# Optimization experiments

Measured on AMD Instinct MI355X. Metric: run time of the kernel, lower is better.

## Reference

```python
import jax, jax.numpy as jnp
import numpy as np

N = 100000      # nodes
E = 1600000     # edges (avg degree 16)
EP = 500000     # pos/neg scored edges
DIN, DH, DOUT = 128, 128, 64


def setup_inputs() -> dict:
    key = jax.random.key(0)
    ks = jax.random.split(key, 8)
    x = jax.random.normal(ks[0], (N, DIN), jnp.float32)
    edge_index = jax.random.randint(ks[1], (2, E), 0, N)
    pos_edge_index = jax.random.randint(ks[2], (2, EP), 0, N)
    neg_edge_index = jax.random.randint(ks[3], (2, EP), 0, N)
    s = lambda k, sh: jax.random.normal(k, sh, jnp.float32) * 0.05
    return dict(
        x=x, edge_index=edge_index,
        pos_edge_index=pos_edge_index, neg_edge_index=neg_edge_index,
        W_l0=s(ks[4], (DIN, DH)), b_l0=jnp.zeros((DH,), jnp.float32), W_r0=s(ks[5], (DIN, DH)),
        W_l1=s(ks[6], (DH, DOUT)), b_l1=jnp.zeros((DOUT,), jnp.float32), W_r1=s(ks[7], (DH, DOUT)),
    )


def sage_conv(h, src, dst, W_l, b_l, W_r):
    # PyG SAGEConv (mean aggr): out_i = W_l @ mean_{j in N(i)} h_j + b_l + W_r @ h_i
    msg = h[src]                                                   # [E, d] gather
    agg = jax.ops.segment_sum(msg, dst, num_segments=h.shape[0])   # [N, d]
    deg = jax.ops.segment_sum(jnp.ones((src.shape[0],), h.dtype), dst, num_segments=h.shape[0])
    mean = agg / jnp.maximum(deg, 1.0)[:, None]
    return mean @ W_l + b_l + h @ W_r


def reference(x, edge_index, pos_edge_index, neg_edge_index,
              W_l0, b_l0, W_r0, W_l1, b_l1, W_r1):
    src, dst = edge_index[0], edge_index[1]
    h = sage_conv(x, src, dst, W_l0, b_l0, W_r0)
    h = jax.nn.relu(h)          # dropout is identity in eval mode
    h = sage_conv(h, src, dst, W_l1, b_l1, W_r1)
    pos_scores = (h[pos_edge_index[0]] * h[pos_edge_index[1]]).sum(axis=1)
    neg_scores = (h[neg_edge_index[0]] * h[neg_edge_index[1]]).sum(axis=1)
    return (pos_scores, neg_scores)
```

## Files before the change

kernel.cpp:

```cpp
#include <hip/hip_runtime.h>

#define NN 100000
#define EE 1600000
#define EPE 500000
#define NBINS 196
#define BCAP 12288
#define EPB 2048
#define NB1 782

typedef short bf8_t __attribute__((ext_vector_type(8)));
typedef float f4_t  __attribute__((ext_vector_type(4)));

__device__ __forceinline__ unsigned short f2bf(float f) {
    unsigned u = __float_as_uint(f);
    unsigned r = (u + 0x7fffu + ((u >> 16) & 1u)) >> 16;
    return (unsigned short)r;
}
__device__ __forceinline__ float bfl(unsigned u) { return __uint_as_float(u << 16); }
__device__ __forceinline__ float bfh(unsigned u) { return __uint_as_float(u & 0xffff0000u); }

__global__ __launch_bounds__(256) void binpass1_k(
    const int* __restrict__ src, const int* __restrict__ dst,
    int* __restrict__ bin_cnt, int* __restrict__ binbuf)
{
    __shared__ int cnt_l[NBINS];
    __shared__ int base_l[NBINS];
    int tid = threadIdx.x;
    int e0 = blockIdx.x * EPB;
    for (int i = tid; i < NBINS; i += 256) cnt_l[i] = 0;
    __syncthreads();

    int pk[8];
    #pragma unroll
    for (int i = 0; i < 8; ++i) {
        int e = e0 + tid + i * 256;
        pk[i] = -1;
        if (e < EE) {
            int b = dst[e] >> 9;
            int r = atomicAdd(&cnt_l[b], 1);
            pk[i] = (b << 16) | r;
        }
    }
    __syncthreads();
    for (int i = tid; i < NBINS; i += 256)
        base_l[i] = atomicAdd(&bin_cnt[i], cnt_l[i]);
    __syncthreads();

    #pragma unroll
    for (int i = 0; i < 8; ++i) {
        int e = e0 + tid + i * 256;
        if (e >= EE) continue;
        int b = pk[i] >> 16, r = pk[i] & 0xFFFF;
        int d = dst[e], s = src[e];
        binbuf[b * BCAP + base_l[b] + r] = ((d & 511) << 17) | s;
    }
}

__global__ __launch_bounds__(256) void binpass2_k(
    const int* __restrict__ binbuf, const int* __restrict__ bin_cnt,
    int* __restrict__ csr, int* __restrict__ row_ptr, float* __restrict__ invd)
{
    __shared__ int deg_l[512];
    __shared__ int off_l[512];
    __shared__ int cur_l[512];
    __shared__ int s[256];
    int tid = threadIdx.x;
    int b = blockIdx.x;
    int lo = b << 9;
    int n_here = min(512, NN - lo);

    int bc = (tid < NBINS) ? bin_cnt[tid] : 0;
    s[tid] = bc;
    __syncthreads();
    #pragma unroll
    for (int off = 1; off < 256; off <<= 1) {
        int t = (tid >= off) ? s[tid - off] : 0;
        __syncthreads();
        s[tid] += t;
        __syncthreads();
    }
    int base = (b == 0) ? 0 : s[b - 1];
    int cnt = bin_cnt[b];
    const int* bb = binbuf + b * BCAP;
    __syncthreads();

    deg_l[tid] = 0; deg_l[tid + 256] = 0;
    __syncthreads();
    for (int i = tid; i < cnt; i += 256)
        atomicAdd(&deg_l[bb[i] >> 17], 1);
    __syncthreads();

    int a0 = deg_l[2 * tid], a1 = deg_l[2 * tid + 1];
    s[tid] = a0 + a1;
    __syncthreads();
    #pragma unroll
    for (int off = 1; off < 256; off <<= 1) {
        int t = (tid >= off) ? s[tid - off] : 0;
        __syncthreads();
        s[tid] += t;
        __syncthreads();
    }
    int excl = s[tid] - (a0 + a1);
    off_l[2 * tid] = excl;
    off_l[2 * tid + 1] = excl + a0;
    cur_l[2 * tid] = excl;
    cur_l[2 * tid + 1] = excl + a0;
    __syncthreads();

    for (int j = tid; j < n_here; j += 256) {
        row_ptr[lo + j] = base + off_l[j];
        invd[lo + j] = 1.0f / fmaxf((float)deg_l[j], 1.0f);
    }
    if (tid == 0 && b == NBINS - 1) row_ptr[NN] = EE;

    for (int i = tid; i < cnt; i += 256) {
        int v = bb[i];
        int dstl = v >> 17, srcv = v & 0x1FFFF;
        int pos = atomicAdd(&cur_l[dstl], 1);
        csr[base + pos] = srcv;
    }
}

__global__ void pack_k(const float* __restrict__ Wl0, const float* __restrict__ Wr0,
                       const float* __restrict__ Wl1, const float* __restrict__ Wr1,
                       const float* __restrict__ bl0, const float* __restrict__ bl1,
                       unsigned short* __restrict__ Bp0, unsigned short* __restrict__ Bp1,
                       float* __restrict__ b0p, float* __restrict__ b1p)
{
    int t = blockIdx.x * 256 + threadIdx.x;
    if (t < 4096) {
        int q = t & 3;
        int n = (t >> 2) & 255;
        int kt = t >> 10;
        unsigned short o[8];
        #pragma unroll
        for (int j = 0; j < 8; ++j) {
            int k = kt * 32 + q * 8 + j;
            float v = (n < 128) ? Wl0[(size_t)k * 128 + n] : Wr0[(size_t)k * 128 + (n - 128)];
            o[j] = f2bf(v);
        }
        uint4 w;
        w.x = (unsigned)o[0] | ((unsigned)o[1] << 16);
        w.y = (unsigned)o[2] | ((unsigned)o[3] << 16);
        w.z = (unsigned)o[4] | ((unsigned)o[5] << 16);
        w.w = (unsigned)o[6] | ((unsigned)o[7] << 16);
        *(uint4*)(Bp0 + (size_t)t * 8) = w;
    } else if (t < 6144) {
        int u = t - 4096;
        int q = u & 3;
        int n = (u >> 2) & 127;
        int kt = u >> 9;
        unsigned short o[8];
        #pragma unroll
        for (int j = 0; j < 8; ++j) {
            int k = kt * 32 + q * 8 + j;
            int c = ((k & 7) << 4) | (k >> 3);
            float v = (n < 64) ? Wl1[(size_t)c * 64 + n] : Wr1[(size_t)c * 64 + (n - 64)];
            o[j] = f2bf(v);
        }
        uint4 w;
        w.x = (unsigned)o[0] | ((unsigned)o[1] << 16);
        w.y = (unsigned)o[2] | ((unsigned)o[3] << 16);
        w.z = (unsigned)o[4] | ((unsigned)o[5] << 16);
        w.w = (unsigned)o[6] | ((unsigned)o[7] << 16);
        *(uint4*)(Bp1 + (size_t)u * 8) = w;
    } else if (t < 6144 + 128) {
        int m = t - 6144;
        b0p[m] = bl0[((m & 7) << 4) | (m >> 3)];
    } else if (t < 6144 + 192) {
        int m = t - 6272;
        b1p[m] = bl1[((m & 3) << 4) | (m >> 2)];
    }
}

template<int NCOLS, int TCOLS, bool AFP32>
__global__ __launch_bounds__(256) void gemm_k(
    const void* __restrict__ Av, const unsigned short* __restrict__ Bp,
    unsigned short* __restrict__ Tout, unsigned short* __restrict__ Rout)
{
    constexpr int NT = NCOLS / 16;
    constexpr int NTH = NCOLS / 32;
    int wave = threadIdx.x >> 6;
    int lane = threadIdx.x & 63;
    int ln = lane & 15, q = lane >> 4;
    int row0 = (blockIdx.x * 4 + wave) * 16;
    if (row0 >= NN) return;
    int arow = row0 + ln;

    f4_t acc[NT];
    #pragma unroll
    for (int nt = 0; nt < NT; ++nt) acc[nt] = (f4_t){0.f, 0.f, 0.f, 0.f};

    #pragma unroll
    for (int kt = 0; kt < 4; ++kt) {
        bf8_t a;
        if (AFP32) {
            const float* ap = (const float*)Av + (size_t)arow * 128 + kt * 32 + q * 8;
            f4_t a0 = *(const f4_t*)ap;
            f4_t a1 = *(const f4_t*)(ap + 4);
            #pragma unroll
            for (int j = 0; j < 4; ++j) {
                a[j]     = (short)f2bf(a0[j]);
                a[4 + j] = (short)f2bf(a1[j]);
            }
        } else {
            a = *(const bf8_t*)((const unsigned short*)Av + (size_t)arow * 128 + kt * 32 + q * 8);
        }
        const unsigned short* bb = Bp + (size_t)kt * NCOLS * 32 + (size_t)ln * 32 + q * 8;
        #pragma unroll
        for (int nt = 0; nt < NT; ++nt) {
            bf8_t b = *(const bf8_t*)(bb + nt * 512);
            acc[nt] = __builtin_amdgcn_mfma_f32_16x16x32_bf16(a, b, acc[nt], 0, 0, 0);
        }
    }

    #pragma unroll
    for (int r = 0; r < 4; ++r) {
        int row = row0 + q * 4 + r;
        if (NTH == 8) {
            uint4 wt, wr;
            wt.x = (unsigned)f2bf(acc[0][r]) | ((unsigned)f2bf(acc[1][r]) << 16);
            wt.y = (unsigned)f2bf(acc[2][r]) | ((unsigned)f2bf(acc[3][r]) << 16);
            wt.z = (unsigned)f2bf(acc[4][r]) | ((unsigned)f2bf(acc[5][r]) << 16);
            wt.w = (unsigned)f2bf(acc[6][r]) | ((unsigned)f2bf(acc[7][r]) << 16);
            wr.x = (unsigned)f2bf(acc[8][r])  | ((unsigned)f2bf(acc[9][r])  << 16);
            wr.y = (unsigned)f2bf(acc[10][r]) | ((unsigned)f2bf(acc[11][r]) << 16);
            wr.z = (unsigned)f2bf(acc[12][r]) | ((unsigned)f2bf(acc[13][r]) << 16);
            wr.w = (unsigned)f2bf(acc[14][r]) | ((unsigned)f2bf(acc[15][r]) << 16);
            *(uint4*)(Tout + (size_t)row * TCOLS + ln * 8) = wt;
            *(uint4*)(Rout + (size_t)row * TCOLS + ln * 8) = wr;
        } else {
            uint2 wt, wr;
            wt.x = (unsigned)f2bf(acc[0][r]) | ((unsigned)f2bf(acc[1][r]) << 16);
            wt.y = (unsigned)f2bf(acc[2][r]) | ((unsigned)f2bf(acc[3][r]) << 16);
            wr.x = (unsigned)f2bf(acc[4][r]) | ((unsigned)f2bf(acc[5][r]) << 16);
            wr.y = (unsigned)f2bf(acc[6][r]) | ((unsigned)f2bf(acc[7][r]) << 16);
            *(uint2*)(Tout + (size_t)row * TCOLS + ln * 4) = wt;
            *(uint2*)(Rout + (size_t)row * TCOLS + ln * 4) = wr;
        }
    }
}

#define ACC8(a, v)                                                          \
    do {                                                                    \
        a[0] += bfl((v).x); a[1] += bfh((v).x);                             \
        a[2] += bfl((v).y); a[3] += bfh((v).y);                             \
        a[4] += bfl((v).z); a[5] += bfh((v).z);                             \
        a[6] += bfl((v).w); a[7] += bfh((v).w);                             \
    } while (0)

template<int LPNS, int WIDTH, bool RELU>
__global__ void gather_fuse_k(const unsigned short* __restrict__ feat,
                              const int* __restrict__ csr, const int* __restrict__ row_ptr,
                              const float* __restrict__ invd,
                              const unsigned short* __restrict__ rterm,
                              const float* __restrict__ bias,
                              unsigned short* __restrict__ hout)
{
    int t = blockIdx.x * 256 + threadIdx.x;
    int node = t >> LPNS;
    int lane = t & ((1 << LPNS) - 1);
    if (node >= NN) return;
    int e = row_ptr[node];
    int e1 = row_ptr[node + 1];
    const unsigned short* fb = feat + (size_t)lane * 8;

    float a0[8] = {0.f, 0.f, 0.f, 0.f, 0.f, 0.f, 0.f, 0.f};
    float a1[8] = {0.f, 0.f, 0.f, 0.f, 0.f, 0.f, 0.f, 0.f};
    for (; e + 3 < e1; e += 4) {
        int s0 = csr[e], s1 = csr[e + 1], s2 = csr[e + 2], s3 = csr[e + 3];
        uint4 v0 = *(const uint4*)(fb + (size_t)s0 * WIDTH);
        uint4 v1 = *(const uint4*)(fb + (size_t)s1 * WIDTH);
        uint4 v2 = *(const uint4*)(fb + (size_t)s2 * WIDTH);
        uint4 v3 = *(const uint4*)(fb + (size_t)s3 * WIDTH);
        ACC8(a0, v0); ACC8(a1, v1); ACC8(a0, v2); ACC8(a1, v3);
    }
    for (; e < e1; ++e) {
        int s0 = csr[e];
        uint4 v0 = *(const uint4*)(fb + (size_t)s0 * WIDTH);
        ACC8(a0, v0);
    }
    float inv = invd[node];
    uint4 rv = *(const uint4*)(rterm + (size_t)node * WIDTH + lane * 8);
    float rr[8] = {bfl(rv.x), bfh(rv.x), bfl(rv.y), bfh(rv.y),
                   bfl(rv.z), bfh(rv.z), bfl(rv.w), bfh(rv.w)};
    f4_t b0 = *(const f4_t*)(bias + lane * 8);
    f4_t b1 = *(const f4_t*)(bias + lane * 8 + 4);
    float o[8];
    #pragma unroll
    for (int j = 0; j < 8; ++j) {
        float bj = (j < 4) ? b0[j] : b1[j - 4];
        float v = (a0[j] + a1[j]) * inv + rr[j] + bj;
        o[j] = RELU ? fmaxf(v, 0.f) : v;
    }
    uint4 w;
    w.x = (unsigned)f2bf(o[0]) | ((unsigned)f2bf(o[1]) << 16);
    w.y = (unsigned)f2bf(o[2]) | ((unsigned)f2bf(o[3]) << 16);
    w.z = (unsigned)f2bf(o[4]) | ((unsigned)f2bf(o[5]) << 16);
    w.w = (unsigned)f2bf(o[6]) | ((unsigned)f2bf(o[7]) << 16);
    *(uint4*)(hout + (size_t)node * WIDTH + lane * 8) = w;
}

__device__ __forceinline__ float dot8(uint4 va, uint4 vb) {
    return bfl(va.x) * bfl(vb.x) + bfh(va.x) * bfh(vb.x)
         + bfl(va.y) * bfl(vb.y) + bfh(va.y) * bfh(vb.y)
         + bfl(va.z) * bfl(vb.z) + bfh(va.z) * bfh(vb.z)
         + bfl(va.w) * bfl(vb.w) + bfh(va.w) * bfh(vb.w);
}

__global__ void score_k(const unsigned short* __restrict__ h2b, const int* __restrict__ pos,
                        const int* __restrict__ neg, float* __restrict__ out) {
    int t = blockIdx.x * 256 + threadIdx.x;
    int g = t >> 3, l = t & 7;
    int eg0 = g * 2;
    if (eg0 >= 2 * EPE) return;
    int eg1 = eg0 + 1;
    int a0i, b0i, a1i, b1i;
    if (eg0 < EPE) { a0i = pos[eg0]; b0i = pos[EPE + eg0]; }
    else { int e2 = eg0 - EPE; a0i = neg[e2]; b0i = neg[EPE + e2]; }
    if (eg1 < EPE) { a1i = pos[eg1]; b1i = pos[EPE + eg1]; }
    else { int e2 = eg1 - EPE; a1i = neg[e2]; b1i = neg[EPE + e2]; }
    const unsigned short* hb = h2b + (size_t)l * 8;
    uint4 va0 = *(const uint4*)(hb + (size_t)a0i * 64);
    uint4 vb0 = *(const uint4*)(hb + (size_t)b0i * 64);
    uint4 va1 = *(const uint4*)(hb + (size_t)a1i * 64);
    uint4 vb1 = *(const uint4*)(hb + (size_t)b1i * 64);
    float p0 = dot8(va0, vb0);
    float p1 = dot8(va1, vb1);
    p0 += __shfl_xor(p0, 1, 8);
    p1 += __shfl_xor(p1, 1, 8);
    p0 += __shfl_xor(p0, 2, 8);
    p1 += __shfl_xor(p1, 2, 8);
    p0 += __shfl_xor(p0, 4, 8);
    p1 += __shfl_xor(p1, 4, 8);
    if (l == 0) { out[eg0] = p0; out[eg1] = p1; }
}

extern "C" void kernel_launch(void* const* d_in, const int* in_sizes, int n_in,
                              void* d_out, int out_size, void* d_ws, size_t ws_size,
                              hipStream_t stream) {
    const float* x   = (const float*)d_in[0];
    const int*   ei  = (const int*)d_in[1];
    const int*   pei = (const int*)d_in[2];
    const int*   nei = (const int*)d_in[3];
    const float* Wl0 = (const float*)d_in[4];
    const float* bl0 = (const float*)d_in[5];
    const float* Wr0 = (const float*)d_in[6];
    const float* Wl1 = (const float*)d_in[7];
    const float* bl1 = (const float*)d_in[8];
    const float* Wr1 = (const float*)d_in[9];
    float* out = (float*)d_out;

    char* ws = (char*)d_ws;
    size_t off = 0;
    auto alloc = [&](size_t bytes) {
        void* p = ws + off;
        off = (off + bytes + 255) & ~(size_t)255;
        return p;
    };
    float* invd     = (float*)alloc((size_t)NN * 4);
    int*   row_ptr  = (int*)  alloc((size_t)(NN + 1) * 4);
    int*   bin_cnt  = (int*)  alloc((size_t)NBINS * 4);
    int*   binbuf   = (int*)  alloc((size_t)NBINS * BCAP * 4);
    int*   csr      = (int*)  alloc((size_t)EE * 4);
    unsigned short* Bp0 = (unsigned short*)alloc((size_t)4096 * 8 * 2);
    unsigned short* Bp1 = (unsigned short*)alloc((size_t)2048 * 8 * 2);
    float* b0p = (float*)alloc(128 * 4);
    float* b1p = (float*)alloc(64 * 4);
    unsigned short* t0  = (unsigned short*)alloc((size_t)NN * 128 * 2);
    unsigned short* r0b = (unsigned short*)alloc((size_t)NN * 128 * 2);
    unsigned short* h1b = (unsigned short*)alloc((size_t)NN * 128 * 2);
    unsigned short* t1  = t0;
    unsigned short* r1b = r0b;
    unsigned short* h2b = h1b;

    const int* src = ei;
    const int* dst = ei + EE;

    hipMemsetAsync(bin_cnt, 0, (size_t)NBINS * 4, stream);

    binpass1_k<<<NB1, 256, 0, stream>>>(src, dst, bin_cnt, binbuf);
    binpass2_k<<<NBINS, 256, 0, stream>>>(binbuf, bin_cnt, csr, row_ptr, invd);

    pack_k<<<25, 256, 0, stream>>>(Wl0, Wr0, Wl1, Wr1, bl0, bl1, Bp0, Bp1, b0p, b1p);

    gemm_k<256, 128, true><<<1563, 256, 0, stream>>>(x, Bp0, t0, r0b);
    gather_fuse_k<4, 128, true><<<(NN * 16 + 255) / 256, 256, 0, stream>>>(
        t0, csr, row_ptr, invd, r0b, b0p, h1b);

    gemm_k<128, 64, false><<<1563, 256, 0, stream>>>(h1b, Bp1, t1, r1b);
    gather_fuse_k<3, 64, false><<<(NN * 8 + 255) / 256, 256, 0, stream>>>(
        t1, csr, row_ptr, invd, r1b, b1p, h2b);

    score_k<<<(EPE * 8 + 255) / 256, 256, 0, stream>>>(h2b, pei, nei, out);
}
```

Baseline: 334.6 us.

## Split node features into 16-column groups for cache-local gathers

Node feature tensors are stored as column groups of 16 bf16 values, laid out group-major across all nodes. Each gather and score block now processes a single group, so the randomly indexed working set per pass shrinks to one slice that can stay in cache. The score kernel accumulates partial dot products with float atomics into an output buffer that is zeroed first. The binning pass also packs the local dst into its register key to avoid reloading dst. The trade-off is re-reading the CSR indices once per group and paying for atomics plus an extra memset.

```diff
diff --git a/kernel.cpp b/kernel.cpp
--- a/kernel.cpp
+++ b/kernel.cpp
@@ -7,6 +7,7 @@
 #define BCAP 12288
 #define EPB 2048
 #define NB1 782
+#define NBG 391
 
 typedef short bf8_t __attribute__((ext_vector_type(8)));
 typedef float f4_t  __attribute__((ext_vector_type(4)));
@@ -18,6 +19,13 @@
 }
 __device__ __forceinline__ float bfl(unsigned u) { return __uint_as_float(u << 16); }
 __device__ __forceinline__ float bfh(unsigned u) { return __uint_as_float(u & 0xffff0000u); }
+
+__device__ __host__ __forceinline__ int c0p(int m) {
+    return ((m & 7) << 4) | (((m >> 4) & 7) << 1) | ((m >> 3) & 1);
+}
+__device__ __host__ __forceinline__ int c1p(int m) {
+    return ((m & 3) << 4) | (((m >> 4) & 3) << 2) | ((m >> 2) & 3);
+}
 
 __global__ __launch_bounds__(256) void binpass1_k(
     const int* __restrict__ src, const int* __restrict__ dst,
@@ -36,9 +44,10 @@
         int e = e0 + tid + i * 256;
         pk[i] = -1;
         if (e < EE) {
-            int b = dst[e] >> 9;
+            int d = dst[e];
+            int b = d >> 9;
             int r = atomicAdd(&cnt_l[b], 1);
-            pk[i] = (b << 16) | r;
+            pk[i] = (b << 20) | ((d & 511) << 11) | r;
         }
     }
     __syncthreads();
@@ -50,9 +59,9 @@
     for (int i = 0; i < 8; ++i) {
         int e = e0 + tid + i * 256;
         if (e >= EE) continue;
-        int b = pk[i] >> 16, r = pk[i] & 0xFFFF;
-        int d = dst[e], s = src[e];
-        binbuf[b * BCAP + base_l[b] + r] = ((d & 511) << 17) | s;
+        int v = pk[i];
+        int b = v >> 20, dl = (v >> 11) & 511, r = v & 2047;
+        binbuf[b * BCAP + base_l[b] + r] = (dl << 17) | src[e];
     }
 }
 
@@ -154,7 +163,7 @@
         #pragma unroll
         for (int j = 0; j < 8; ++j) {
             int k = kt * 32 + q * 8 + j;
-            int c = ((k & 7) << 4) | (k >> 3);
+            int c = c0p(k);
             float v = (n < 64) ? Wl1[(size_t)c * 64 + n] : Wr1[(size_t)c * 64 + (n - 64)];
             o[j] = f2bf(v);
         }
@@ -166,14 +175,14 @@
         *(uint4*)(Bp1 + (size_t)u * 8) = w;
     } else if (t < 6144 + 128) {
         int m = t - 6144;
-        b0p[m] = bl0[((m & 7) << 4) | (m >> 3)];
+        b0p[m] = bl0[c0p(m)];
     } else if (t < 6144 + 192) {
         int m = t - 6272;
-        b1p[m] = bl1[((m & 3) << 4) | (m >> 2)];
-    }
-}
-
-template<int NCOLS, int TCOLS, bool AFP32>
+        b1p[m] = bl1[c1p(m)];
+    }
+}
+
+template<int NCOLS, bool AFP32>
 __global__ __launch_bounds__(256) void gemm_k(
     const void* __restrict__ Av, const unsigned short* __restrict__ Bp,
     unsigned short* __restrict__ Tout, unsigned short* __restrict__ Rout)
@@ -204,7 +213,9 @@
                 a[4 + j] = (short)f2bf(a1[j]);
             }
         } else {
-            a = *(const bf8_t*)((const unsigned short*)Av + (size_t)arow * 128 + kt * 32 + q * 8);
+            int g = kt * 2 + (q >> 1);
+            int slot = (q & 1) * 8;
+            a = *(const bf8_t*)((const unsigned short*)Av + ((size_t)g * NN + arow) * 16 + slot);
         }
         const unsigned short* bb = Bp + (size_t)kt * NCOLS * 32 + (size_t)ln * 32 + q * 8;
         #pragma unroll
@@ -218,6 +229,7 @@
     for (int r = 0; r < 4; ++r) {
         int row = row0 + q * 4 + r;
         if (NTH == 8) {
+            size_t tb = ((size_t)(ln >> 1) * NN + row) * 16 + (ln & 1) * 8;
             uint4 wt, wr;
             wt.x = (unsigned)f2bf(acc[0][r]) | ((unsigned)f2bf(acc[1][r]) << 16);
             wt.y = (unsigned)f2bf(acc[2][r]) | ((unsigned)f2bf(acc[3][r]) << 16);
@@ -227,78 +239,97 @@
             wr.y = (unsigned)f2bf(acc[10][r]) | ((unsigned)f2bf(acc[11][r]) << 16);
             wr.z = (unsigned)f2bf(acc[12][r]) | ((unsigned)f2bf(acc[13][r]) << 16);
             wr.w = (unsigned)f2bf(acc[14][r]) | ((unsigned)f2bf(acc[15][r]) << 16);
-            *(uint4*)(Tout + (size_t)row * TCOLS + ln * 8) = wt;
-            *(uint4*)(Rout + (size_t)row * TCOLS + ln * 8) = wr;
+            *(uint4*)(Tout + tb) = wt;
+            *(uint4*)(Rout + tb) = wr;
         } else {
+            size_t tb = ((size_t)(ln >> 2) * NN + row) * 16 + (ln & 3) * 4;
             uint2 wt, wr;
             wt.x = (unsigned)f2bf(acc[0][r]) | ((unsigned)f2bf(acc[1][r]) << 16);
             wt.y = (unsigned)f2bf(acc[2][r]) | ((unsigned)f2bf(acc[3][r]) << 16);
             wr.x = (unsigned)f2bf(acc[4][r]) | ((unsigned)f2bf(acc[5][r]) << 16);
             wr.y = (unsigned)f2bf(acc[6][r]) | ((unsigned)f2bf(acc[7][r]) << 16);
-            *(uint2*)(Tout + (size_t)row * TCOLS + ln * 4) = wt;
-            *(uint2*)(Rout + (size_t)row * TCOLS + ln * 4) = wr;
-        }
-    }
-}
-
-#define ACC8(a, v)                                                          \
-    do {                                                                    \
-        a[0] += bfl((v).x); a[1] += bfh((v).x);                             \
-        a[2] += bfl((v).y); a[3] += bfh((v).y);                             \
-        a[4] += bfl((v).z); a[5] += bfh((v).z);                             \
-        a[6] += bfl((v).w); a[7] += bfh((v).w);                             \
-    } while (0)
-
-template<int LPNS, int WIDTH, bool RELU>
-__global__ void gather_fuse_k(const unsigned short* __restrict__ feat,
-                              const int* __restrict__ csr, const int* __restrict__ row_ptr,
-                              const float* __restrict__ invd,
-                              const unsigned short* __restrict__ rterm,
-                              const float* __restrict__ bias,
-                              unsigned short* __restrict__ hout)
-{
-    int t = blockIdx.x * 256 + threadIdx.x;
-    int node = t >> LPNS;
-    int lane = t & ((1 << LPNS) - 1);
+            *(uint2*)(Tout + tb) = wt;
+            *(uint2*)(Rout + tb) = wr;
+        }
+    }
+}
+
+__device__ __forceinline__ void acc8(float* a, uint4 v) {
+    a[0] += bfl(v.x); a[1] += bfh(v.x);
+    a[2] += bfl(v.y); a[3] += bfh(v.y);
+    a[4] += bfl(v.z); a[5] += bfh(v.z);
+    a[6] += bfl(v.w); a[7] += bfh(v.w);
+}
+__device__ __forceinline__ void unp8(float* a, uint4 v) {
+    a[0] = bfl(v.x); a[1] = bfh(v.x);
+    a[2] = bfl(v.y); a[3] = bfh(v.y);
+    a[4] = bfl(v.z); a[5] = bfh(v.z);
+    a[6] = bfl(v.w); a[7] = bfh(v.w);
+}
+
+template<int NGROUPS, bool RELU>
+__global__ __launch_bounds__(256) void gather_fuse_k(
+    const unsigned short* __restrict__ tg, const int* __restrict__ csr,
+    const int* __restrict__ row_ptr, const float* __restrict__ invd,
+    const unsigned short* __restrict__ rg, const float* __restrict__ biasp,
+    unsigned short* __restrict__ outg)
+{
+    int g = blockIdx.x % NGROUPS;
+    int node = (blockIdx.x / NGROUPS) * 256 + threadIdx.x;
     if (node >= NN) return;
+    const unsigned short* base = tg + (size_t)g * NN * 16;
     int e = row_ptr[node];
     int e1 = row_ptr[node + 1];
-    const unsigned short* fb = feat + (size_t)lane * 8;
-
-    float a0[8] = {0.f, 0.f, 0.f, 0.f, 0.f, 0.f, 0.f, 0.f};
-    float a1[8] = {0.f, 0.f, 0.f, 0.f, 0.f, 0.f, 0.f, 0.f};
-    for (; e + 3 < e1; e += 4) {
-        int s0 = csr[e], s1 = csr[e + 1], s2 = csr[e + 2], s3 = csr[e + 3];
-        uint4 v0 = *(const uint4*)(fb + (size_t)s0 * WIDTH);
-        uint4 v1 = *(const uint4*)(fb + (size_t)s1 * WIDTH);
-        uint4 v2 = *(const uint4*)(fb + (size_t)s2 * WIDTH);
-        uint4 v3 = *(const uint4*)(fb + (size_t)s3 * WIDTH);
-        ACC8(a0, v0); ACC8(a1, v1); ACC8(a0, v2); ACC8(a1, v3);
-    }
-    for (; e < e1; ++e) {
+
+    float a0[16], a1[16];
+    #pragma unroll
+    for (int j = 0; j < 16; ++j) { a0[j] = 0.f; a1[j] = 0.f; }
+
+    for (; e + 1 < e1; e += 2) {
+        int s0 = csr[e], s1 = csr[e + 1];
+        const unsigned short* p0 = base + (size_t)s0 * 16;
+        const unsigned short* p1 = base + (size_t)s1 * 16;
+        uint4 v00 = *(const uint4*)p0;
+        uint4 v01 = *(const uint4*)(p0 + 8);
+        uint4 v10 = *(const uint4*)p1;
+        uint4 v11 = *(const uint4*)(p1 + 8);
+        acc8(a0, v00); acc8(a0 + 8, v01);
+        acc8(a1, v10); acc8(a1 + 8, v11);
+    }
+    if (e < e1) {
         int s0 = csr[e];
-        uint4 v0 = *(const uint4*)(fb + (size_t)s0 * WIDTH);
-        ACC8(a0, v0);
-    }
+        const unsigned short* p0 = base + (size_t)s0 * 16;
+        uint4 v00 = *(const uint4*)p0;
+        uint4 v01 = *(const uint4*)(p0 + 8);
+        acc8(a0, v00); acc8(a0 + 8, v01);
+    }
+
     float inv = invd[node];
-    uint4 rv = *(const uint4*)(rterm + (size_t)node * WIDTH + lane * 8);
-    float rr[8] = {bfl(rv.x), bfh(rv.x), bfl(rv.y), bfh(rv.y),
-                   bfl(rv.z), bfh(rv.z), bfl(rv.w), bfh(rv.w)};
-    f4_t b0 = *(const f4_t*)(bias + lane * 8);
-    f4_t b1 = *(const f4_t*)(bias + lane * 8 + 4);
-    float o[8];
-    #pragma unroll
-    for (int j = 0; j < 8; ++j) {
-        float bj = (j < 4) ? b0[j] : b1[j - 4];
-        float v = (a0[j] + a1[j]) * inv + rr[j] + bj;
-        o[j] = RELU ? fmaxf(v, 0.f) : v;
-    }
-    uint4 w;
-    w.x = (unsigned)f2bf(o[0]) | ((unsigned)f2bf(o[1]) << 16);
-    w.y = (unsigned)f2bf(o[2]) | ((unsigned)f2bf(o[3]) << 16);
-    w.z = (unsigned)f2bf(o[4]) | ((unsigned)f2bf(o[5]) << 16);
-    w.w = (unsigned)f2bf(o[6]) | ((unsigned)f2bf(o[7]) << 16);
-    *(uint4*)(hout + (size_t)node * WIDTH + lane * 8) = w;
+    const unsigned short* rp = rg + ((size_t)g * NN + node) * 16;
+    uint4 rv0 = *(const uint4*)rp;
+    uint4 rv1 = *(const uint4*)(rp + 8);
+    float rr[16];
+    unp8(rr, rv0); unp8(rr + 8, rv1);
+    const float* bp = biasp + g * 16;
+
+    unsigned short o[16];
+    #pragma unroll
+    for (int j = 0; j < 16; ++j) {
+        float v = (a0[j] + a1[j]) * inv + rr[j] + bp[j];
+        o[j] = f2bf(RELU ? fmaxf(v, 0.f) : v);
+    }
+    uint4 w0, w1;
+    w0.x = (unsigned)o[0]  | ((unsigned)o[1]  << 16);
+    w0.y = (unsigned)o[2]  | ((unsigned)o[3]  << 16);
+    w0.z = (unsigned)o[4]  | ((unsigned)o[5]  << 16);
+    w0.w = (unsigned)o[6]  | ((unsigned)o[7]  << 16);
+    w1.x = (unsigned)o[8]  | ((unsigned)o[9]  << 16);
+    w1.y = (unsigned)o[10] | ((unsigned)o[11] << 16);
+    w1.z = (unsigned)o[12] | ((unsigned)o[13] << 16);
+    w1.w = (unsigned)o[14] | ((unsigned)o[15] << 16);
+    unsigned short* op = outg + ((size_t)g * NN + node) * 16;
+    *(uint4*)op = w0;
+    *(uint4*)(op + 8) = w1;
 }
 
 __device__ __forceinline__ float dot8(uint4 va, uint4 vb) {
@@ -308,32 +339,25 @@
          + bfl(va.w) * bfl(vb.w) + bfh(va.w) * bfh(vb.w);
 }
 
-__global__ void score_k(const unsigned short* __restrict__ h2b, const int* __restrict__ pos,
-                        const int* __restrict__ neg, float* __restrict__ out) {
-    int t = blockIdx.x * 256 + threadIdx.x;
-    int g = t >> 3, l = t & 7;
-    int eg0 = g * 2;
-    if (eg0 >= 2 * EPE) return;
-    int eg1 = eg0 + 1;
-    int a0i, b0i, a1i, b1i;
-    if (eg0 < EPE) { a0i = pos[eg0]; b0i = pos[EPE + eg0]; }
-    else { int e2 = eg0 - EPE; a0i = neg[e2]; b0i = neg[EPE + e2]; }
-    if (eg1 < EPE) { a1i = pos[eg1]; b1i = pos[EPE + eg1]; }
-    else { int e2 = eg1 - EPE; a1i = neg[e2]; b1i = neg[EPE + e2]; }
-    const unsigned short* hb = h2b + (size_t)l * 8;
-    uint4 va0 = *(const uint4*)(hb + (size_t)a0i * 64);
-    uint4 vb0 = *(const uint4*)(hb + (size_t)b0i * 64);
-    uint4 va1 = *(const uint4*)(hb + (size_t)a1i * 64);
-    uint4 vb1 = *(const uint4*)(hb + (size_t)b1i * 64);
-    float p0 = dot8(va0, vb0);
-    float p1 = dot8(va1, vb1);
-    p0 += __shfl_xor(p0, 1, 8);
-    p1 += __shfl_xor(p1, 1, 8);
-    p0 += __shfl_xor(p0, 2, 8);
-    p1 += __shfl_xor(p1, 2, 8);
-    p0 += __shfl_xor(p0, 4, 8);
-    p1 += __shfl_xor(p1, 4, 8);
-    if (l == 0) { out[eg0] = p0; out[eg1] = p1; }
+__global__ __launch_bounds__(256) void score_k(
+    const unsigned short* __restrict__ h2q, const int* __restrict__ pos,
+    const int* __restrict__ neg, float* __restrict__ out)
+{
+    int qd = blockIdx.x & 3;
+    int eg = (blockIdx.x >> 2) * 256 + threadIdx.x;
+    if (eg >= 2 * EPE) return;
+    int a, b;
+    if (eg < EPE) { a = pos[eg]; b = pos[EPE + eg]; }
+    else { int e2 = eg - EPE; a = neg[e2]; b = neg[EPE + e2]; }
+    const unsigned short* hb = h2q + (size_t)qd * NN * 16;
+    const unsigned short* pa = hb + (size_t)a * 16;
+    const unsigned short* pb = hb + (size_t)b * 16;
+    uint4 va0 = *(const uint4*)pa;
+    uint4 va1 = *(const uint4*)(pa + 8);
+    uint4 vb0 = *(const uint4*)pb;
+    uint4 vb1 = *(const uint4*)(pb + 8);
+    float p = dot8(va0, vb0) + dot8(va1, vb1);
+    atomicAdd(&out[eg], p);
 }
 
 extern "C" void kernel_launch(void* const* d_in, const int* in_sizes, int n_in,
@@ -367,30 +391,31 @@
     unsigned short* Bp1 = (unsigned short*)alloc((size_t)2048 * 8 * 2);
     float* b0p = (float*)alloc(128 * 4);
     float* b1p = (float*)alloc(64 * 4);
-    unsigned short* t0  = (unsigned short*)alloc((size_t)NN * 128 * 2);
-    unsigned short* r0b = (unsigned short*)alloc((size_t)NN * 128 * 2);
-    unsigned short* h1b = (unsigned short*)alloc((size_t)NN * 128 * 2);
-    unsigned short* t1  = t0;
-    unsigned short* r1b = r0b;
-    unsigned short* h2b = h1b;
+    unsigned short* t0g = (unsigned short*)alloc((size_t)8 * NN * 16 * 2);
+    unsigned short* r0g = (unsigned short*)alloc((size_t)8 * NN * 16 * 2);
+    unsigned short* h1g = (unsigned short*)alloc((size_t)8 * NN * 16 * 2);
+    unsigned short* t1g = t0g;
+    unsigned short* r1g = r0g;
+    unsigned short* h2q = h1g;
 
     const int* src = ei;
     const int* dst = ei + EE;
 
     hipMemsetAsync(bin_cnt, 0, (size_t)NBINS * 4, stream);
+    hipMemsetAsync(out, 0, (size_t)2 * EPE * 4, stream);
 
     binpass1_k<<<NB1, 256, 0, stream>>>(src, dst, bin_cnt, binbuf);
     binpass2_k<<<NBINS, 256, 0, stream>>>(binbuf, bin_cnt, csr, row_ptr, invd);
 
     pack_k<<<25, 256, 0, stream>>>(Wl0, Wr0, Wl1, Wr1, bl0, bl1, Bp0, Bp1, b0p, b1p);
 
-    gemm_k<256, 128, true><<<1563, 256, 0, stream>>>(x, Bp0, t0, r0b);
-    gather_fuse_k<4, 128, true><<<(NN * 16 + 255) / 256, 256, 0, stream>>>(
-        t0, csr, row_ptr, invd, r0b, b0p, h1b);
-
-    gemm_k<128, 64, false><<<1563, 256, 0, stream>>>(h1b, Bp1, t1, r1b);
-    gather_fuse_k<3, 64, false><<<(NN * 8 + 255) / 256, 256, 0, stream>>>(
-        t1, csr, row_ptr, invd, r1b, b1p, h2b);
-
-    score_k<<<(EPE * 8 + 255) / 256, 256, 0, stream>>>(h2b, pei, nei, out);
-}
+    gemm_k<256, true><<<1563, 256, 0, stream>>>(x, Bp0, t0g, r0g);
+    gather_fuse_k<8, true><<<8 * NBG, 256, 0, stream>>>(
+        t0g, csr, row_ptr, invd, r0g, b0p, h1g);
+
+    gemm_k<128, false><<<1563, 256, 0, stream>>>(h1g, Bp1, t1g, r1g);
+    gather_fuse_k<4, false><<<4 * NBG, 256, 0, stream>>>(
+        t1g, csr, row_ptr, invd, r1g, b1p, h2q);
+
+    score_k<<<4 * ((2 * EPE + 255) / 256), 256, 0, stream>>>(h2q, pei, nei, out);
+}
```

Measured after the change: 483.5 us. 1.44x slower.

## Store neighbor-transformed features as FP8 to halve gather traffic

Applied to the files above, without the earlier changes.

The GEMM now writes the W_l-transformed features that get gathered per edge as FP8 E4M3 instead of bf16, and the gather kernels load and decode 8-byte chunks. This halves the bytes fetched in the dominant random-access edge gather. It also drops the separate memset by zeroing bin counts inside pack_k, launched first, and packs the local dst into the binning key so dst is not reloaded. FP8 reduces the precision of the aggregated messages, which risks accuracy-tolerance failures.

```diff
diff --git a/kernel.cpp b/kernel.cpp
--- a/kernel.cpp
+++ b/kernel.cpp
@@ -10,6 +10,7 @@
 
 typedef short bf8_t __attribute__((ext_vector_type(8)));
 typedef float f4_t  __attribute__((ext_vector_type(4)));
+typedef float f2v  __attribute__((ext_vector_type(2)));
 
 __device__ __forceinline__ unsigned short f2bf(float f) {
     unsigned u = __float_as_uint(f);
@@ -18,6 +19,43 @@
 }
 __device__ __forceinline__ float bfl(unsigned u) { return __uint_as_float(u << 16); }
 __device__ __forceinline__ float bfh(unsigned u) { return __uint_as_float(u & 0xffff0000u); }
+
+#if __has_builtin(__builtin_amdgcn_cvt_pk_fp8_f32) && __has_builtin(__builtin_amdgcn_cvt_pk_f32_fp8)
+__device__ __forceinline__ unsigned pk4_fp8(float a0, float a1, float a2, float a3) {
+    int w = 0;
+    w = __builtin_amdgcn_cvt_pk_fp8_f32(a0, a1, w, false);
+    w = __builtin_amdgcn_cvt_pk_fp8_f32(a2, a3, w, true);
+    return (unsigned)w;
+}
+__device__ __forceinline__ void accf8(float* a, uint2 v) {
+    f2v p0 = __builtin_amdgcn_cvt_pk_f32_fp8((int)v.x, false);
+    f2v p1 = __builtin_amdgcn_cvt_pk_f32_fp8((int)v.x, true);
+    f2v p2 = __builtin_amdgcn_cvt_pk_f32_fp8((int)v.y, false);
+    f2v p3 = __builtin_amdgcn_cvt_pk_f32_fp8((int)v.y, true);
+    a[0] += p0.x; a[1] += p0.y; a[2] += p1.x; a[3] += p1.y;
+    a[4] += p2.x; a[5] += p2.y; a[6] += p3.x; a[7] += p3.y;
+}
+#else
+#include <hip/hip_fp8.h>
+__device__ __forceinline__ unsigned pk4_fp8(float a0, float a1, float a2, float a3) {
+    unsigned r;
+    r  = (unsigned)__hip_cvt_float_to_fp8(a0, __HIP_SATFINITE, __HIP_E4M3);
+    r |= (unsigned)__hip_cvt_float_to_fp8(a1, __HIP_SATFINITE, __HIP_E4M3) << 8;
+    r |= (unsigned)__hip_cvt_float_to_fp8(a2, __HIP_SATFINITE, __HIP_E4M3) << 16;
+    r |= (unsigned)__hip_cvt_float_to_fp8(a3, __HIP_SATFINITE, __HIP_E4M3) << 24;
+    return r;
+}
+__device__ __forceinline__ float dec1_fp8(unsigned b) {
+    __hip_fp8_e4m3 h; h.__x = (__hip_fp8_storage_t)(b & 0xff);
+    return (float)h;
+}
+__device__ __forceinline__ void accf8(float* a, uint2 v) {
+    a[0] += dec1_fp8(v.x); a[1] += dec1_fp8(v.x >> 8);
+    a[2] += dec1_fp8(v.x >> 16); a[3] += dec1_fp8(v.x >> 24);
+    a[4] += dec1_fp8(v.y); a[5] += dec1_fp8(v.y >> 8);
+    a[6] += dec1_fp8(v.y >> 16); a[7] += dec1_fp8(v.y >> 24);
+}
+#endif
 
 __global__ __launch_bounds__(256) void binpass1_k(
     const int* __restrict__ src, const int* __restrict__ dst,
@@ -36,9 +74,10 @@
         int e = e0 + tid + i * 256;
         pk[i] = -1;
         if (e < EE) {
-            int b = dst[e] >> 9;
+            int d = dst[e];
+            int b = d >> 9;
             int r = atomicAdd(&cnt_l[b], 1);
-            pk[i] = (b << 16) | r;
+            pk[i] = (b << 20) | ((d & 511) << 11) | r;
         }
     }
     __syncthreads();
@@ -50,9 +89,9 @@
     for (int i = 0; i < 8; ++i) {
         int e = e0 + tid + i * 256;
         if (e >= EE) continue;
-        int b = pk[i] >> 16, r = pk[i] & 0xFFFF;
-        int d = dst[e], s = src[e];
-        binbuf[b * BCAP + base_l[b] + r] = ((d & 511) << 17) | s;
+        int v = pk[i];
+        int b = v >> 20, dl = (v >> 11) & 511, r = v & 2047;
+        binbuf[b * BCAP + base_l[b] + r] = (dl << 17) | src[e];
     }
 }
 
@@ -125,9 +164,11 @@
                        const float* __restrict__ Wl1, const float* __restrict__ Wr1,
                        const float* __restrict__ bl0, const float* __restrict__ bl1,
                        unsigned short* __restrict__ Bp0, unsigned short* __restrict__ Bp1,
-                       float* __restrict__ b0p, float* __restrict__ b1p)
+                       float* __restrict__ b0p, float* __restrict__ b1p,
+                       int* __restrict__ bin_cnt)
 {
     int t = blockIdx.x * 256 + threadIdx.x;
+    if (t < NBINS) bin_cnt[t] = 0;
     if (t < 4096) {
         int q = t & 3;
         int n = (t >> 2) & 255;
@@ -173,13 +214,14 @@
     }
 }
 
-template<int NCOLS, int TCOLS, bool AFP32>
+template<int NCOLS, bool AFP32>
 __global__ __launch_bounds__(256) void gemm_k(
     const void* __restrict__ Av, const unsigned short* __restrict__ Bp,
-    unsigned short* __restrict__ Tout, unsigned short* __restrict__ Rout)
+    unsigned char* __restrict__ Tout, unsigned short* __restrict__ Rout)
 {
     constexpr int NT = NCOLS / 16;
     constexpr int NTH = NCOLS / 32;
+    constexpr int HC = NCOLS / 2;
     int wave = threadIdx.x >> 6;
     int lane = threadIdx.x & 63;
     int ln = lane & 15, q = lane >> 4;
@@ -218,74 +260,72 @@
     for (int r = 0; r < 4; ++r) {
         int row = row0 + q * 4 + r;
         if (NTH == 8) {
-            uint4 wt, wr;
-            wt.x = (unsigned)f2bf(acc[0][r]) | ((unsigned)f2bf(acc[1][r]) << 16);
-            wt.y = (unsigned)f2bf(acc[2][r]) | ((unsigned)f2bf(acc[3][r]) << 16);
-            wt.z = (unsigned)f2bf(acc[4][r]) | ((unsigned)f2bf(acc[5][r]) << 16);
-            wt.w = (unsigned)f2bf(acc[6][r]) | ((unsigned)f2bf(acc[7][r]) << 16);
+            uint2 wt;
+            wt.x = pk4_fp8(acc[0][r], acc[1][r], acc[2][r], acc[3][r]);
+            wt.y = pk4_fp8(acc[4][r], acc[5][r], acc[6][r], acc[7][r]);
+            *(uint2*)(Tout + (size_t)row * HC + ln * 8) = wt;
+            uint4 wr;
             wr.x = (unsigned)f2bf(acc[8][r])  | ((unsigned)f2bf(acc[9][r])  << 16);
             wr.y = (unsigned)f2bf(acc[10][r]) | ((unsigned)f2bf(acc[11][r]) << 16);
             wr.z = (unsigned)f2bf(acc[12][r]) | ((unsigned)f2bf(acc[13][r]) << 16);
             wr.w = (unsigned)f2bf(acc[14][r]) | ((unsigned)f2bf(acc[15][r]) << 16);
-            *(uint4*)(Tout + (size_t)row * TCOLS + ln * 8) = wt;
-            *(uint4*)(Rout + (size_t)row * TCOLS + ln * 8) = wr;
+            *(uint4*)(Rout + (size_t)row * HC + ln * 8) = wr;
         } else {
-            uint2 wt, wr;
-            wt.x = (unsigned)f2bf(acc[0][r]) | ((unsigned)f2bf(acc[1][r]) << 16);
-            wt.y = (unsigned)f2bf(acc[2][r]) | ((unsigned)f2bf(acc[3][r]) << 16);
+            unsigned wt = pk4_fp8(acc[0][r], acc[1][r], acc[2][r], acc[3][r]);
+            *(unsigned*)(Tout + (size_t)row * HC + ln * 4) = wt;
+            uint2 wr;
             wr.x = (unsigned)f2bf(acc[4][r]) | ((unsigned)f2bf(acc[5][r]) << 16);
             wr.y = (unsigned)f2bf(acc[6][r]) | ((unsigned)f2bf(acc[7][r]) << 16);
-            *(uint2*)(Tout + (size_t)row * TCOLS + ln * 4) = wt;
-            *(uint2*)(Rout + (size_t)row * TCOLS + ln * 4) = wr;
-        }
-    }
-}
-
-#define ACC8(a, v)                                                          \
-    do {                                                                    \
-        a[0] += bfl((v).x); a[1] += bfh((v).x);                             \
-        a[2] += bfl((v).y); a[3] += bfh((v).y);                             \
-        a[4] += bfl((v).z); a[5] += bfh((v).z);                             \
-        a[6] += bfl((v).w); a[7] += bfh((v).w);                             \
-    } while (0)
-
-template<int LPNS, int WIDTH, bool RELU>
-__global__ void gather_fuse_k(const unsigned short* __restrict__ feat,
-                              const int* __restrict__ csr, const int* __restrict__ row_ptr,
-                              const float* __restrict__ invd,
-                              const unsigned short* __restrict__ rterm,
-                              const float* __restrict__ bias,
-                              unsigned short* __restrict__ hout)
-{
+            *(uint2*)(Rout + (size_t)row * HC + ln * 4) = wr;
+        }
+    }
+}
+
+__device__ __forceinline__ void unp8(float* a, uint4 v) {
+    a[0] = bfl(v.x); a[1] = bfh(v.x);
+    a[2] = bfl(v.y); a[3] = bfh(v.y);
+    a[4] = bfl(v.z); a[5] = bfh(v.z);
+    a[6] = bfl(v.w); a[7] = bfh(v.w);
+}
+
+template<int LPNS, bool RELU>
+__global__ __launch_bounds__(256) void gather_fuse_k(
+    const unsigned char* __restrict__ tq, const int* __restrict__ csr,
+    const int* __restrict__ row_ptr, const float* __restrict__ invd,
+    const unsigned short* __restrict__ rg, const float* __restrict__ biasp,
+    unsigned short* __restrict__ hout)
+{
+    constexpr int STRIDE = 8 << LPNS;
     int t = blockIdx.x * 256 + threadIdx.x;
     int node = t >> LPNS;
     int lane = t & ((1 << LPNS) - 1);
     if (node >= NN) return;
     int e = row_ptr[node];
     int e1 = row_ptr[node + 1];
-    const unsigned short* fb = feat + (size_t)lane * 8;
+    const unsigned char* fb = tq + lane * 8;
 
     float a0[8] = {0.f, 0.f, 0.f, 0.f, 0.f, 0.f, 0.f, 0.f};
     float a1[8] = {0.f, 0.f, 0.f, 0.f, 0.f, 0.f, 0.f, 0.f};
     for (; e + 3 < e1; e += 4) {
         int s0 = csr[e], s1 = csr[e + 1], s2 = csr[e + 2], s3 = csr[e + 3];
-        uint4 v0 = *(const uint4*)(fb + (size_t)s0 * WIDTH);
-        uint4 v1 = *(const uint4*)(fb + (size_t)s1 * WIDTH);
-        uint4 v2 = *(const uint4*)(fb + (size_t)s2 * WIDTH);
-        uint4 v3 = *(const uint4*)(fb + (size_t)s3 * WIDTH);
-        ACC8(a0, v0); ACC8(a1, v1); ACC8(a0, v2); ACC8(a1, v3);
+        uint2 v0 = *(const uint2*)(fb + (size_t)s0 * STRIDE);
+        uint2 v1 = *(const uint2*)(fb + (size_t)s1 * STRIDE);
+        uint2 v2 = *(const uint2*)(fb + (size_t)s2 * STRIDE);
+        uint2 v3 = *(const uint2*)(fb + (size_t)s3 * STRIDE);
+        accf8(a0, v0); accf8(a1, v1); accf8(a0, v2); accf8(a1, v3);
     }
     for (; e < e1; ++e) {
         int s0 = csr[e];
-        uint4 v0 = *(const uint4*)(fb + (size_t)s0 * WIDTH);
-        ACC8(a0, v0);
-    }
+        uint2 v0 = *(const uint2*)(fb + (size_t)s0 * STRIDE);
+        accf8(a0, v0);
+    }
+
     float inv = invd[node];
-    uint4 rv = *(const uint4*)(rterm + (size_t)node * WIDTH + lane * 8);
-    float rr[8] = {bfl(rv.x), bfh(rv.x), bfl(rv.y), bfh(rv.y),
-                   bfl(rv.z), bfh(rv.z), bfl(rv.w), bfh(rv.w)};
-    f4_t b0 = *(const f4_t*)(bias + lane * 8);
-    f4_t b1 = *(const f4_t*)(bias + lane * 8 + 4);
+    uint4 rv = *(const uint4*)(rg + (size_t)node * STRIDE + lane * 8);
+    float rr[8];
+    unp8(rr, rv);
+    f4_t b0 = *(const f4_t*)(biasp + lane * 8);
+    f4_t b1 = *(const f4_t*)(biasp + lane * 8 + 4);
     float o[8];
     #pragma unroll
     for (int j = 0; j < 8; ++j) {
@@ -298,7 +338,7 @@
     w.y = (unsigned)f2bf(o[2]) | ((unsigned)f2bf(o[3]) << 16);
     w.z = (unsigned)f2bf(o[4]) | ((unsigned)f2bf(o[5]) << 16);
     w.w = (unsigned)f2bf(o[6]) | ((unsigned)f2bf(o[7]) << 16);
-    *(uint4*)(hout + (size_t)node * WIDTH + lane * 8) = w;
+    *(uint4*)(hout + (size_t)node * STRIDE + lane * 8) = w;
 }
 
 __device__ __forceinline__ float dot8(uint4 va, uint4 vb) {
@@ -308,8 +348,10 @@
          + bfl(va.w) * bfl(vb.w) + bfh(va.w) * bfh(vb.w);
 }
 
-__global__ void score_k(const unsigned short* __restrict__ h2b, const int* __restrict__ pos,
-                        const int* __restrict__ neg, float* __restrict__ out) {
+__global__ __launch_bounds__(256) void score_k(
+    const unsigned short* __restrict__ h2b, const int* __restrict__ pos,
+    const int* __restrict__ neg, float* __restrict__ out)
+{
     int t = blockIdx.x * 256 + threadIdx.x;
     int g = t >> 3, l = t & 7;
     int eg0 = g * 2;
@@ -367,30 +409,27 @@
     unsigned short* Bp1 = (unsigned short*)alloc((size_t)2048 * 8 * 2);
     float* b0p = (float*)alloc(128 * 4);
     float* b1p = (float*)alloc(64 * 4);
-    unsigned short* t0  = (unsigned short*)alloc((size_t)NN * 128 * 2);
+    unsigned char*  t0q = (unsigned char*) alloc((size_t)NN * 128);
     unsigned short* r0b = (unsigned short*)alloc((size_t)NN * 128 * 2);
     unsigned short* h1b = (unsigned short*)alloc((size_t)NN * 128 * 2);
-    unsigned short* t1  = t0;
+    unsigned char*  t1q = t0q;
     unsigned short* r1b = r0b;
     unsigned short* h2b = h1b;
 
     const int* src = ei;
     const int* dst = ei + EE;
 
-    hipMemsetAsync(bin_cnt, 0, (size_t)NBINS * 4, stream);
-
+    pack_k<<<25, 256, 0, stream>>>(Wl0, Wr0, Wl1, Wr1, bl0, bl1, Bp0, Bp1, b0p, b1p, bin_cnt);
     binpass1_k<<<NB1, 256, 0, stream>>>(src, dst, bin_cnt, binbuf);
     binpass2_k<<<NBINS, 256, 0, stream>>>(binbuf, bin_cnt, csr, row_ptr, invd);
 
-    pack_k<<<25, 256, 0, stream>>>(Wl0, Wr0, Wl1, Wr1, bl0, bl1, Bp0, Bp1, b0p, b1p);
-
-    gemm_k<256, 128, true><<<1563, 256, 0, stream>>>(x, Bp0, t0, r0b);
-    gather_fuse_k<4, 128, true><<<(NN * 16 + 255) / 256, 256, 0, stream>>>(
-        t0, csr, row_ptr, invd, r0b, b0p, h1b);
-
-    gemm_k<128, 64, false><<<1563, 256, 0, stream>>>(h1b, Bp1, t1, r1b);
-    gather_fuse_k<3, 64, false><<<(NN * 8 + 255) / 256, 256, 0, stream>>>(
-        t1, csr, row_ptr, invd, r1b, b1p, h2b);
+    gemm_k<256, true><<<1563, 256, 0, stream>>>(x, Bp0, t0q, r0b);
+    gather_fuse_k<4, true><<<(NN * 16 + 255) / 256, 256, 0, stream>>>(
+        t0q, csr, row_ptr, invd, r0b, b0p, h1b);
+
+    gemm_k<128, false><<<1563, 256, 0, stream>>>(h1b, Bp1, t1q, r1b);
+    gather_fuse_k<3, false><<<(NN * 8 + 255) / 256, 256, 0, stream>>>(
+        t1q, csr, row_ptr, invd, r1b, b1p, h2b);
 
     score_k<<<(EPE * 8 + 255) / 256, 256, 0, stream>>>(h2b, pei, nei, out);
 }
```

Measured after the change: 299.0 us. 1.12x faster.
